# Kernel optimization log

Hardware: AMD Instinct MI355X
Metric: run time of the kernel (lower is better)

The kernel has to match this reference:

```python
import jax, jax.numpy as jnp
import numpy as np

NUM_CLASSES = 1000
EMB_DIM = 768
BATCH = 16384
EPS = 1e-8  # torch F.cosine_similarity eps


def setup_inputs() -> dict:
    key = jax.random.key(0)
    k1, k2, k3, k4 = jax.random.split(key, 4)
    embeddings = jax.random.normal(k1, (BATCH, EMB_DIM), dtype=jnp.float32)
    logits = jax.random.normal(k2, (BATCH, NUM_CLASSES), dtype=jnp.float32)
    targets = jax.random.randint(k3, (BATCH,), 0, NUM_CLASSES, dtype=jnp.int64 if jax.config.jax_enable_x64 else jnp.int32)
    centroids = jax.random.normal(k4, (NUM_CLASSES, EMB_DIM), dtype=jnp.float32)
    u = jnp.ones((1,), dtype=jnp.float32)
    return {"embeddings": embeddings, "logits": logits, "targets": targets,
            "centroids": centroids, "u": u}


def _cosine_sim(embeddings, centroids):
    # torch cosine_similarity: x / max(||x||, eps); formulated as normalize + GEMM
    en = embeddings / jnp.maximum(jnp.linalg.norm(embeddings, axis=1, keepdims=True), EPS)
    cn = centroids / jnp.maximum(jnp.linalg.norm(centroids, axis=1, keepdims=True), EPS)
    return jnp.einsum('nd,cd->nc', en, cn)  # [N, C]


def reference(embeddings, logits, targets, centroids, u):
    n_classes = centroids.shape[0]
    # cross entropy (mean reduction)
    logp = jax.nn.log_softmax(logits, axis=1)
    ce_loss = -jnp.mean(jnp.take_along_axis(logp, targets[:, None], axis=1))

    sim = _cosine_sim(embeddings, centroids)            # [N, C]
    soft_labels = jax.nn.softmax(sim, axis=1)           # [N, C]

    hard_one_hot = jax.nn.one_hot(targets, n_classes, dtype=jnp.float32)
    similarity_to_target = jnp.sum(soft_labels * hard_one_hot, axis=1)  # [N]
    discount = 1.0 - similarity_to_target
    reg_term = jnp.mean(discount) * u                   # shape (1,)

    # mse_loss(hard_one_hot, soft_labels.detach()) -- soft_labels detached
    dist_reg = jnp.mean((hard_one_hot - jax.lax.stop_gradient(soft_labels)) ** 2)

    return ce_loss + dist_reg + reg_term                # shape (1,)
```

## Files before the change

kernel.cpp:

```cpp
#include <hip/hip_runtime.h>
#include <hip/hip_bf16.h>
#include <stdint.h>

#define BATCH 16384
#define NCLS 1000
#define NPAD 1024
#define EMB 768
#define KT 12
#define BM 128
#define BN 256
#define ABYTES 8192
#define BUFB 24576
#define GEMM_BLKS 512
#define CE_BLKS 4096

typedef __attribute__((ext_vector_type(4))) float f32x4;
typedef long v2i64 __attribute__((ext_vector_type(2)));

#define GLOAD16(g, l) __builtin_amdgcn_global_load_lds(              \
    (const __attribute__((address_space(1))) unsigned int*)(g),       \
    (__attribute__((address_space(3))) unsigned int*)(l), 16, 0, 0)

__device__ __forceinline__ float d4(float4 v) {
    return v.x*v.x + v.y*v.y + v.z*v.z + v.w*v.w;
}
__device__ __forceinline__ float e4(float4 v) {
    return __expf(v.x) + __expf(v.y) + __expf(v.z) + __expf(v.w);
}
__device__ __forceinline__ unsigned int pk8(float4 v, float s) {
    int p = 0;
    p = __builtin_amdgcn_cvt_pk_fp8_f32(v.x * s, v.y * s, p, false);
    p = __builtin_amdgcn_cvt_pk_fp8_f32(v.z * s, v.w * s, p, true);
    return (unsigned int)p;
}

__global__ __launch_bounds__(192) void prep_ec(
    const float* __restrict__ emb, const float* __restrict__ cent,
    unsigned int* __restrict__ en8, unsigned int* __restrict__ cn8)
{
    __shared__ float ssp[3];
    const int b    = blockIdx.x;
    const int tid  = threadIdx.x;
    const int w    = tid >> 6;
    const int lane = tid & 63;

    const bool isC = b >= BATCH;
    const int row  = isC ? b - BATCH : b;
    const bool valid = !isC || row < NCLS;

    const float4* src = isC ? (const float4*)(cent + (size_t)row * EMB)
                            : (const float4*)(emb + (size_t)row * EMB);
    float4 v = (valid) ? src[tid] : make_float4(0.f, 0.f, 0.f, 0.f);

    float ss = d4(v);
    #pragma unroll
    for (int m = 1; m < 64; m <<= 1) ss += __shfl_xor(ss, m, 64);
    if (lane == 0) ssp[w] = ss;
    __syncthreads();
    const float tot = ssp[0] + ssp[1] + ssp[2];
    const float sc = valid ? (1.0f / fmaxf(sqrtf(tot), 1e-8f)) : 0.0f;

    unsigned int* op = (isC ? cn8 : en8) + (size_t)row * (EMB / 4);
    op[tid] = pk8(v, sc);
}

__global__ __launch_bounds__(256) void ce_kernel(
    const float* __restrict__ logits, const int* __restrict__ targets,
    float* __restrict__ ce_row)
{
    const int row  = blockIdx.x * 4 + (threadIdx.x >> 6);
    const int lane = threadIdx.x & 63;
    const float* rp = logits + (size_t)row * NCLS;
    const float4* r4 = (const float4*)rp;

    float4 v0 = r4[lane];
    float4 v1 = r4[lane + 64];
    float4 v2 = r4[lane + 128];
    const bool has = lane < 58;
    float4 v3 = has ? r4[lane + 192] : v0;

    float s = e4(v0) + e4(v1) + e4(v2);
    if (has) s += e4(v3);

    #pragma unroll
    for (int m = 1; m < 64; m <<= 1) s += __shfl_xor(s, m, 64);

    if (lane == 0) {
        float xt = rp[targets[row]];
        ce_row[row] = __logf(s) - xt;
    }
}

__global__ __launch_bounds__(256, 2) void gemm_kernel(
    const uint8_t* __restrict__ en8, const uint8_t* __restrict__ cn8,
    const int* __restrict__ targets,
    float* __restrict__ partZ, float* __restrict__ partS2,
    float* __restrict__ et_out)
{
    __shared__ __align__(128) uint8_t lds[2][BUFB];

    const int bid  = blockIdx.x;
    const int tid  = threadIdx.x;
    const int lane = tid & 63;
    const int warp = tid >> 6;

    const int g   = bid & 7;
    const int s   = bid >> 3;
    const int mb  = g * 16 + (s >> 2);
    const int nb  = s & 3;
    const int R0  = mb * BM;
    const int Nc0 = nb * BN;
    const int wr  = warp >> 1;
    const int wc  = warp & 1;
    const int l15 = lane & 15;
    const int rq  = lane >> 4;

    const int csw  = ((tid & 3) * 16) ^ (((tid >> 3) & 3) << 4);
    const int srow = tid >> 2;
    size_t asrc[2], bsrc[4];
    #pragma unroll
    for (int j = 0; j < 2; ++j) asrc[j] = (size_t)(R0  + j * 64 + srow) * EMB + csw;
    #pragma unroll
    for (int j = 0; j < 4; ++j) bsrc[j] = (size_t)(Nc0 + j * 64 + srow) * EMB + csw;
    const uint8_t* enb = en8;
    const uint8_t* cnb = cn8;

#define STAGE(b, kt) do { const size_t ko = (size_t)(kt) * 64;               \
    _Pragma("unroll") for (int j = 0; j < 2; ++j)                            \
        GLOAD16(enb + asrc[j] + ko, &lds[b][j * 4096 + tid * 16]);           \
    _Pragma("unroll") for (int j = 0; j < 4; ++j)                            \
        GLOAD16(cnb + bsrc[j] + ko, &lds[b][ABYTES + j * 4096 + tid * 16]);  \
} while (0)

    const int cx   = (rq * 16) ^ (((l15 >> 1) & 3) << 4);
    const int aoff = (wr * 64 + l15) * 64 + cx;
    const int boff = ABYTES + (wc * 128 + l15) * 64 + cx;

    f32x4 acc[4][8];
    #pragma unroll
    for (int m = 0; m < 4; ++m)
        #pragma unroll
        for (int n = 0; n < 8; ++n) acc[m][n] = (f32x4){0.f, 0.f, 0.f, 0.f};

    STAGE(0, 0);
    __syncthreads();

    for (int kt = 0; kt < KT; ++kt) {
        const int buf = kt & 1;
        if (kt + 1 < KT) STAGE(buf ^ 1, kt + 1);
        const uint8_t* L = &lds[buf][0];
        v2i64 af[4], bf[8];
        #pragma unroll
        for (int m = 0; m < 4; ++m) af[m] = *(const v2i64*)(L + aoff + m * 1024);
        #pragma unroll
        for (int n = 0; n < 8; ++n) bf[n] = *(const v2i64*)(L + boff + n * 1024);
        #pragma unroll
        for (int kk = 0; kk < 2; ++kk)
            #pragma unroll
            for (int m = 0; m < 4; ++m)
                #pragma unroll
                for (int n = 0; n < 8; ++n)
                    acc[m][n] = __builtin_amdgcn_mfma_f32_16x16x32_fp8_fp8(
                        bf[n][kk], af[m][kk], acc[m][n], 0, 0, 0);
        __syncthreads();
    }
#undef STAGE

    const int plane = nb * 2 + wc;
    #pragma unroll
    for (int m = 0; m < 4; ++m) {
        const int row = R0 + wr * 64 + m * 16 + l15;
        const int t   = targets[row];
        float z = 0.f, s2 = 0.f;
        #pragma unroll
        for (int n = 0; n < 8; ++n) {
            const int cb = Nc0 + wc * 128 + n * 16 + rq * 4;
            #pragma unroll
            for (int r = 0; r < 4; ++r) {
                const bool valid = (cb + r) < NCLS;
                float e = valid ? __expf(acc[m][n][r]) : 0.f;
                z += e; s2 += e * e;
                if (cb + r == t) et_out[row] = e;
            }
        }
        z  += __shfl_xor(z, 16, 64);  z  += __shfl_xor(z, 32, 64);
        s2 += __shfl_xor(s2, 16, 64); s2 += __shfl_xor(s2, 32, 64);
        if (rq == 0) {
            partZ [(size_t)plane * BATCH + row] = z;
            partS2[(size_t)plane * BATCH + row] = s2;
        }
    }
}

__global__ __launch_bounds__(256) void finalize1(
    const float* __restrict__ partZ, const float* __restrict__ partS2,
    const float* __restrict__ et_out, const float* __restrict__ ce_row,
    const float* __restrict__ u, float* __restrict__ fpart)
{
    __shared__ float red[4];
    const int row  = blockIdx.x * 256 + threadIdx.x;
    const int lane = threadIdx.x & 63;
    float z = 0.f, s2 = 0.f;
    #pragma unroll
    for (int i = 0; i < 8; ++i) {
        z  += partZ [(size_t)i * BATCH + row];
        s2 += partS2[(size_t)i * BATCH + row];
    }
    float et = et_out[row];
    float invz = 1.0f / z;
    float pt = et * invz;
    float c = (s2 * invz * invz - 2.0f * pt + 1.0f) * (1.0f / ((float)BATCH * (float)NCLS))
            + (1.0f - pt) * u[0] * (1.0f / (float)BATCH)
            + ce_row[row] * (1.0f / (float)BATCH);
    #pragma unroll
    for (int m = 1; m < 64; m <<= 1) c += __shfl_xor(c, m, 64);
    if (lane == 0) red[threadIdx.x >> 6] = c;
    __syncthreads();
    if (threadIdx.x == 0) fpart[blockIdx.x] = red[0] + red[1] + red[2] + red[3];
}

__global__ __launch_bounds__(64) void finalize2(
    const float* __restrict__ fpart, float* __restrict__ out)
{
    const int lane = threadIdx.x;
    float s = fpart[lane];
    #pragma unroll
    for (int m = 1; m < 64; m <<= 1) s += __shfl_xor(s, m, 64);
    if (lane == 0) out[0] = s;
}

extern "C" void kernel_launch(void* const* d_in, const int* in_sizes, int n_in,
                              void* d_out, int out_size, void* d_ws, size_t ws_size,
                              hipStream_t stream) {
    const float* emb       = (const float*)d_in[0];
    const float* logits    = (const float*)d_in[1];
    const int*   targets   = (const int*)d_in[2];
    const float* centroids = (const float*)d_in[3];
    const float* u         = (const float*)d_in[4];
    float* out = (float*)d_out;

    uint8_t* en8  = (uint8_t*)d_ws;
    uint8_t* cn8  = en8 + (size_t)BATCH * EMB;
    float* partZ  = (float*)(cn8 + (size_t)NPAD * EMB);
    float* partS2 = partZ + 8 * BATCH;
    float* et_out = partS2 + 8 * BATCH;
    float* ce_row = et_out + BATCH;
    float* fpart  = ce_row + BATCH;

    prep_ec<<<BATCH + NPAD, 192, 0, stream>>>(emb, centroids,
                                              (unsigned int*)en8, (unsigned int*)cn8);
    ce_kernel<<<CE_BLKS, 256, 0, stream>>>(logits, targets, ce_row);
    gemm_kernel<<<GEMM_BLKS, 256, 0, stream>>>(en8, cn8, targets, partZ, partS2, et_out);
    finalize1<<<BATCH / 256, 256, 0, stream>>>(partZ, partS2, et_out, ce_row, u, fpart);
    finalize2<<<1, 64, 0, stream>>>(fpart, out);
}
```

Before: 54.26 us.

## Fuse normalization prep and cross-entropy kernels into one launch with nontemporal loads

Merges the embedding/centroid FP8 normalization kernel and the cross-entropy row kernel into a single launch whose block index selects the work. The normalization now assigns one wave per row, so the reduction is wave-local and needs no LDS or __syncthreads. All streaming reads go through nontemporal loads. This removes one kernel launch and its tail, and lets the two memory-bound phases share the device, at the cost of more branching in one kernel.

```diff
diff --git a/kernel.cpp b/kernel.cpp
--- a/kernel.cpp
+++ b/kernel.cpp
@@ -12,83 +12,84 @@
 #define ABYTES 8192
 #define BUFB 24576
 #define GEMM_BLKS 512
-#define CE_BLKS 4096
 
 typedef __attribute__((ext_vector_type(4))) float f32x4;
+typedef float f4v __attribute__((ext_vector_type(4)));
 typedef long v2i64 __attribute__((ext_vector_type(2)));
 
 #define GLOAD16(g, l) __builtin_amdgcn_global_load_lds(              \
     (const __attribute__((address_space(1))) unsigned int*)(g),       \
     (__attribute__((address_space(3))) unsigned int*)(l), 16, 0, 0)
 
-__device__ __forceinline__ float d4(float4 v) {
+__device__ __forceinline__ f4v ntl(const float* p) {
+    return __builtin_nontemporal_load((const f4v*)p);
+}
+__device__ __forceinline__ float d4v(f4v v) {
     return v.x*v.x + v.y*v.y + v.z*v.z + v.w*v.w;
 }
-__device__ __forceinline__ float e4(float4 v) {
+__device__ __forceinline__ float e4v(f4v v) {
     return __expf(v.x) + __expf(v.y) + __expf(v.z) + __expf(v.w);
 }
-__device__ __forceinline__ unsigned int pk8(float4 v, float s) {
+__device__ __forceinline__ unsigned int pk8v(f4v v, float s) {
     int p = 0;
     p = __builtin_amdgcn_cvt_pk_fp8_f32(v.x * s, v.y * s, p, false);
     p = __builtin_amdgcn_cvt_pk_fp8_f32(v.z * s, v.w * s, p, true);
     return (unsigned int)p;
 }
 
-__global__ __launch_bounds__(192) void prep_ec(
+__global__ __launch_bounds__(256) void prep_ce(
     const float* __restrict__ emb, const float* __restrict__ cent,
-    unsigned int* __restrict__ en8, unsigned int* __restrict__ cn8)
-{
-    __shared__ float ssp[3];
+    const float* __restrict__ logits, const int* __restrict__ targets,
+    unsigned int* __restrict__ en8, unsigned int* __restrict__ cn8,
+    float* __restrict__ ce_row)
+{
     const int b    = blockIdx.x;
-    const int tid  = threadIdx.x;
-    const int w    = tid >> 6;
-    const int lane = tid & 63;
-
-    const bool isC = b >= BATCH;
-    const int row  = isC ? b - BATCH : b;
-    const bool valid = !isC || row < NCLS;
-
-    const float4* src = isC ? (const float4*)(cent + (size_t)row * EMB)
-                            : (const float4*)(emb + (size_t)row * EMB);
-    float4 v = (valid) ? src[tid] : make_float4(0.f, 0.f, 0.f, 0.f);
-
-    float ss = d4(v);
+    const int lane = threadIdx.x & 63;
+    const int warp = threadIdx.x >> 6;
+
+    if (b >= 4352) {
+        const int row = (b - 4352) * 4 + warp;
+        const float* rp = logits + (size_t)row * NCLS;
+        f4v v0 = ntl(rp + lane * 4);
+        f4v v1 = ntl(rp + (lane + 64) * 4);
+        f4v v2 = ntl(rp + (lane + 128) * 4);
+        const bool has = lane < 58;
+        f4v v3 = has ? ntl(rp + (lane + 192) * 4) : v0;
+        float s = e4v(v0) + e4v(v1) + e4v(v2);
+        if (has) s += e4v(v3);
+        #pragma unroll
+        for (int m = 1; m < 64; m <<= 1) s += __shfl_xor(s, m, 64);
+        if (lane == 0) {
+            float xt = rp[targets[row]];
+            ce_row[row] = __logf(s) - xt;
+        }
+        return;
+    }
+
+    const float* in; unsigned int* outp; int row, nvalid;
+    if (b < 4096) { row = b * 4 + warp;          in = emb;  outp = en8; nvalid = BATCH; }
+    else          { row = (b - 4096) * 4 + warp; in = cent; outp = cn8; nvalid = NCLS; }
+
+    f4v vals[3];
+    #pragma unroll
+    for (int i = 0; i < 3; ++i) vals[i] = (f4v){0.f, 0.f, 0.f, 0.f};
+    float ss = 0.f;
+    if (row < nvalid) {
+        const float* rp = in + (size_t)row * EMB;
+        #pragma unroll
+        for (int i = 0; i < 3; ++i) {
+            vals[i] = ntl(rp + (lane + 64 * i) * 4);
+            ss += d4v(vals[i]);
+        }
+    }
     #pragma unroll
     for (int m = 1; m < 64; m <<= 1) ss += __shfl_xor(ss, m, 64);
-    if (lane == 0) ssp[w] = ss;
-    __syncthreads();
-    const float tot = ssp[0] + ssp[1] + ssp[2];
-    const float sc = valid ? (1.0f / fmaxf(sqrtf(tot), 1e-8f)) : 0.0f;
-
-    unsigned int* op = (isC ? cn8 : en8) + (size_t)row * (EMB / 4);
-    op[tid] = pk8(v, sc);
-}
-
-__global__ __launch_bounds__(256) void ce_kernel(
-    const float* __restrict__ logits, const int* __restrict__ targets,
-    float* __restrict__ ce_row)
-{
-    const int row  = blockIdx.x * 4 + (threadIdx.x >> 6);
-    const int lane = threadIdx.x & 63;
-    const float* rp = logits + (size_t)row * NCLS;
-    const float4* r4 = (const float4*)rp;
-
-    float4 v0 = r4[lane];
-    float4 v1 = r4[lane + 64];
-    float4 v2 = r4[lane + 128];
-    const bool has = lane < 58;
-    float4 v3 = has ? r4[lane + 192] : v0;
-
-    float s = e4(v0) + e4(v1) + e4(v2);
-    if (has) s += e4(v3);
-
-    #pragma unroll
-    for (int m = 1; m < 64; m <<= 1) s += __shfl_xor(s, m, 64);
-
-    if (lane == 0) {
-        float xt = rp[targets[row]];
-        ce_row[row] = __logf(s) - xt;
-    }
+    float scale = (row < nvalid) ? (1.0f / fmaxf(sqrtf(ss), 1e-8f)) : 0.0f;
+
+    unsigned int* op = outp + (size_t)row * (EMB / 4);
+    #pragma unroll
+    for (int i = 0; i < 3; ++i)
+        op[lane + 64 * i] = pk8v(vals[i], scale);
 }
 
 __global__ __launch_bounds__(256, 2) void gemm_kernel(
@@ -247,9 +248,8 @@
     float* ce_row = et_out + BATCH;
     float* fpart  = ce_row + BATCH;
 
-    prep_ec<<<BATCH + NPAD, 192, 0, stream>>>(emb, centroids,
-                                              (unsigned int*)en8, (unsigned int*)cn8);
-    ce_kernel<<<CE_BLKS, 256, 0, stream>>>(logits, targets, ce_row);
+    prep_ce<<<8448, 256, 0, stream>>>(emb, centroids, logits, targets,
+                                      (unsigned int*)en8, (unsigned int*)cn8, ce_row);
     gemm_kernel<<<GEMM_BLKS, 256, 0, stream>>>(en8, cn8, targets, partZ, partS2, et_out);
     finalize1<<<BATCH / 256, 256, 0, stream>>>(partZ, partS2, et_out, ce_row, u, fpart);
     finalize2<<<1, 64, 0, stream>>>(fpart, out);
```

Result: no change. 54.96 us (+1.3%).
